# Kernel tuning notes

Measured on AMD Instinct MI355X. Metric: run time of the kernel, lower is better.

Reference implementation:

```python
import math
import jax, jax.numpy as jnp
import numpy as np

D_MODEL = 1024
NUM_HEADS = 16
HEAD_DIM = D_MODEL // NUM_HEADS
THETA = 10000.0
MAX_SEQ_LEN = 2048
BATCH = 4
SEQ = 2048


def _rope_tables():
    # angles[i, j] = i / theta**(2j/d_k), shapes [max_seq_len, head_dim//2]
    i = jnp.arange(MAX_SEQ_LEN, dtype=jnp.float32)
    k = jnp.arange(0, HEAD_DIM, 2, dtype=jnp.float32) / HEAD_DIM
    angles = i[:, None] * (1.0 / (THETA ** k))[None, :]
    return jnp.cos(angles), jnp.sin(angles)


def _apply_rope(x, token_positions, cos_tab, sin_tab):
    # x: [b, h, s, d_k]; token_positions: [s]
    b, h, s, dk = x.shape
    xr = x.reshape(b, h, s, dk // 2, 2)
    x0, x1 = xr[..., 0], xr[..., 1]
    cos_pos = cos_tab[token_positions]  # [s, dk//2]
    sin_pos = sin_tab[token_positions]
    x0_rot = x0 * cos_pos - x1 * sin_pos
    x1_rot = x0 * sin_pos + x1 * cos_pos
    return jnp.stack([x0_rot, x1_rot], axis=-1).reshape(x.shape)


def setup_inputs() -> dict:
    key = jax.random.key(0)
    k1, k2, k3 = jax.random.split(key, 3)
    std_qkv = math.sqrt(2.0 / (D_MODEL + 3 * D_MODEL))
    std_o = math.sqrt(2.0 / (D_MODEL + D_MODEL))
    return {
        "x": jax.random.normal(k1, (BATCH, SEQ, D_MODEL), dtype=jnp.float32),
        "token_positions": jnp.arange(SEQ, dtype=jnp.int64) if jax.config.jax_enable_x64 else jnp.arange(SEQ, dtype=jnp.int32),
        "qkv_w": jax.random.normal(k2, (3 * D_MODEL, D_MODEL), dtype=jnp.float32) * std_qkv,
        "o_w": jax.random.normal(k3, (D_MODEL, D_MODEL), dtype=jnp.float32) * std_o,
    }


def reference(x, token_positions, qkv_w, o_w):
    b, s, _ = x.shape
    cos_tab, sin_tab = _rope_tables()
    # fused QKV projection: [b, s, 3*d_model]
    qkv = jnp.einsum('bsd,ed->bse', x, qkv_w)
    qkv = qkv.reshape(b, s, 3, NUM_HEADS, HEAD_DIM)
    q = jnp.transpose(qkv[:, :, 0], (0, 2, 1, 3))  # [b, h, s, hd]
    k = jnp.transpose(qkv[:, :, 1], (0, 2, 1, 3))
    v = jnp.transpose(qkv[:, :, 2], (0, 2, 1, 3))
    q = _apply_rope(q, token_positions, cos_tab, sin_tab)
    k = _apply_rope(k, token_positions, cos_tab, sin_tab)
    # causal mask and eager softmax attention (full [b,h,s,s] scores)
    scores = jnp.einsum('bhnk,bhmk->bhnm', q, k) / math.sqrt(HEAD_DIM)
    causal = jnp.tril(jnp.ones((s, s), dtype=bool))
    scores = jnp.where(causal, scores, -jnp.inf)
    attn = jax.nn.softmax(scores, axis=-1)
    ctx = jnp.einsum('bhnm,bhmv->bhnv', attn, v)
    ctx = jnp.transpose(ctx, (0, 2, 1, 3)).reshape(b, s, D_MODEL)
    return jnp.einsum('bsd,ed->bse', ctx, o_w)
```

## Files before the change

### kernel.cpp

```cpp
#include <hip/hip_runtime.h>


#define DM   1024
#define NH   16
#define HD   64
#define SEQL 2048
#define BATCH 4
#define QKV_ELEMS 8388608

using short8 = __attribute__((ext_vector_type(8))) short;
using f32x4  = __attribute__((ext_vector_type(4))) float;
typedef unsigned short u16;

#define WAIT_VM(n) __builtin_amdgcn_s_waitcnt(0x0F70 | (n))
#define BARRIER()  __builtin_amdgcn_s_barrier()

__device__ __forceinline__ u16 f2bf(float f) {
    unsigned u = __builtin_bit_cast(unsigned, f);
    u += 0x7fffu + ((u >> 16) & 1u);
    return (u16)(u >> 16);
}
__device__ __forceinline__ float bf2f(u16 h) {
    unsigned u = ((unsigned)h) << 16;
    return __builtin_bit_cast(float, u);
}
__device__ __forceinline__ unsigned pk2bf(float a, float b) {
    return (unsigned)f2bf(a) | ((unsigned)f2bf(b) << 16);
}
__device__ __forceinline__ float fexp2(float x) {
#if __has_builtin(__builtin_amdgcn_exp2f)
    return __builtin_amdgcn_exp2f(x);
#else
    return __expf(x * 0.6931471805599453f);
#endif
}

__device__ __forceinline__ void load16(const void* g, void* l) {
    __builtin_amdgcn_global_load_lds(
        (__attribute__((address_space(1))) unsigned int*)(unsigned long long)g,
        (__attribute__((address_space(3))) unsigned int*)(unsigned int)(unsigned long long)l,
        16, 0, 0);
}

__global__ __launch_bounds__(256) void prep(const float* __restrict__ x, u16* __restrict__ xb,
                                            const float* __restrict__ qw, u16* __restrict__ wb,
                                            const float* __restrict__ ow, u16* __restrict__ owb,
                                            float* __restrict__ cost, float* __restrict__ sint) {
    int bx = blockIdx.x;
    if (bx < 12288) {
        const float* in; u16* out; int i;
        if (bx < 8192)       { in = x;  out = xb;  i = bx * 256 + threadIdx.x; }
        else if (bx < 11264) { in = qw; out = wb;  i = (bx - 8192) * 256 + threadIdx.x; }
        else                 { in = ow; out = owb; i = (bx - 11264) * 256 + threadIdx.x; }
        float4 v = ((const float4*)in)[i];
        uint2 o;
        o.x = pk2bf(v.x, v.y);
        o.y = pk2bf(v.z, v.w);
        ((uint2*)out)[i] = o;
    } else {
        int t = (bx - 12288) * 256 + threadIdx.x;
        int j = t & 31, pos = t >> 5;
        float freq = exp2f((float)j * (-2.0f / 64.0f) * 13.287712379549449f);
        float ang = (float)pos * freq;
        cost[t] = cosf(ang);
        sint[t] = sinf(ang);
    }
}

__device__ __forceinline__ void gemm128_core(const u16* __restrict__ A,
                                             const u16* __restrict__ B,
                                             int K, int m0, int n0,
                                             u16* As, u16* Bs, f32x4 acc[4][4]) {
    int tid = threadIdx.x, w = tid >> 6, l = tid & 63;
    int l15 = l & 15, l4 = l >> 4;
    int wm = w >> 1, wn = w & 1;
    int r0 = 32 * w + (l >> 2);
    int gblk = ((l & 3) ^ ((l >> 4) & 3)) * 8;
    const u16* gA0 = A + (size_t)(m0 + r0) * K + gblk;
    const u16* gA1 = gA0 + (size_t)16 * K;
    const u16* gB0 = B + (size_t)(n0 + r0) * K + gblk;
    const u16* gB1 = gB0 + (size_t)16 * K;
    char* ldsA = (char*)As + 2048 * w;
    char* ldsB = (char*)Bs + 2048 * w;
    int fo = ((l4 ^ (l15 >> 2)) & 3) * 16;
    f32x4 z = {0.f, 0.f, 0.f, 0.f};
#pragma unroll
    for (int i = 0; i < 4; ++i)
#pragma unroll
        for (int j = 0; j < 4; ++j) acc[i][j] = z;
    int nk = K >> 5;
#pragma unroll
    for (int t = 0; t < 2; ++t) {
        int ko = t << 5, nb = t * 8192;
        load16(gA0 + ko, ldsA + nb); load16(gA1 + ko, ldsA + nb + 1024);
        load16(gB0 + ko, ldsB + nb); load16(gB1 + ko, ldsB + nb + 1024);
    }
    int buf = 0;
    for (int kt = 0; kt < nk; ++kt) {
        if (kt < nk - 1) WAIT_VM(4); else WAIT_VM(0);
        BARRIER();
        if (kt + 2 < nk) {
            int ko = (kt + 2) << 5;
            int nb = 8192 * ((buf + 2) % 3);
            load16(gA0 + ko, ldsA + nb); load16(gA1 + ko, ldsA + nb + 1024);
            load16(gB0 + ko, ldsB + nb); load16(gB1 + ko, ldsB + nb + 1024);
        }
        const char* bA = (const char*)As + 8192 * buf;
        const char* bB = (const char*)Bs + 8192 * buf;
        short8 a[4], b[4];
#pragma unroll
        for (int i = 0; i < 4; ++i)
            a[i] = *(const short8*)(bA + (64 * wm + 16 * i + l15) * 64 + fo);
#pragma unroll
        for (int j = 0; j < 4; ++j)
            b[j] = *(const short8*)(bB + (64 * wn + 16 * j + l15) * 64 + fo);
#pragma unroll
        for (int i = 0; i < 4; ++i)
#pragma unroll
            for (int j = 0; j < 4; ++j)
                acc[i][j] = __builtin_amdgcn_mfma_f32_16x16x32_bf16(a[i], b[j], acc[i][j], 0, 0, 0);
        buf = (buf + 1) % 3;
    }
}

__global__ __launch_bounds__(256) void gemm_qkv(const u16* __restrict__ xb,
                                                const u16* __restrict__ wb,
                                                u16* __restrict__ qkv,
                                                u16* __restrict__ vt) {
    __shared__ __align__(16) u16 As[3 * 128 * 32], Bs[3 * 128 * 32];
    f32x4 acc[4][4];
    int m0 = blockIdx.y * 128, n0 = blockIdx.x * 128;
    gemm128_core(xb, wb, DM, m0, n0, As, Bs, acc);
    int l = threadIdx.x & 63, w = threadIdx.x >> 6;
    int l15 = l & 15, l4 = l >> 4;
    int wm = w >> 1, wn = w & 1;
    if (blockIdx.x >= 16) {
#pragma unroll
        for (int j = 0; j < 4; ++j) {
            int nV = (n0 - 2048) + 64 * wn + 16 * j + l15;
            int h = nV >> 6, d = nV & 63;
#pragma unroll
            for (int i = 0; i < 4; ++i) {
                int sb = m0 + 64 * wm + 16 * i + 4 * l4;
                int b = sb >> 11, s = sb & 2047;
                uint2 pk;
                pk.x = pk2bf(acc[i][j][0], acc[i][j][1]);
                pk.y = pk2bf(acc[i][j][2], acc[i][j][3]);
                *(uint2*)&vt[((size_t)(b * 16 + h) * HD + d) * SEQL + s] = pk;
            }
        }
    } else {
#pragma unroll
        for (int j = 0; j < 4; ++j) {
            int n = n0 + 64 * wn + 16 * j + l15;
            int which = n >> 10, h = (n >> 6) & 15, d = n & 63;
            u16* base = qkv + (size_t)which * QKV_ELEMS;
#pragma unroll
            for (int i = 0; i < 4; ++i) {
#pragma unroll
                for (int r = 0; r < 4; ++r) {
                    int m = m0 + 64 * wm + 16 * i + 4 * l4 + r;
                    int b = m >> 11, s = m & 2047;
                    base[((size_t)(b * 16 + h) * SEQL + s) * HD + d] = f2bf(acc[i][j][r]);
                }
            }
        }
    }
}

__global__ __launch_bounds__(256) void gemm_out(const u16* __restrict__ ctx,
                                                const u16* __restrict__ owb,
                                                float* __restrict__ out) {
    __shared__ __align__(16) u16 As[3 * 128 * 32], Bs[3 * 128 * 32];
    f32x4 acc[4][4];
    int m0 = blockIdx.y * 128, n0 = blockIdx.x * 128;
    gemm128_core(ctx, owb, DM, m0, n0, As, Bs, acc);
    int l = threadIdx.x & 63, w = threadIdx.x >> 6;
    int l15 = l & 15, l4 = l >> 4;
    int wm = w >> 1, wn = w & 1;
#pragma unroll
    for (int i = 0; i < 4; ++i) {
        int mb = m0 + 64 * wm + 16 * i + 4 * l4;
#pragma unroll
        for (int j = 0; j < 4; ++j) {
            int n = n0 + 64 * wn + 16 * j + l15;
#pragma unroll
            for (int r = 0; r < 4; ++r)
                out[(size_t)(mb + r) * DM + n] = acc[i][j][r];
        }
    }
}

__global__ __launch_bounds__(256) void rope_apply(unsigned int* __restrict__ qk,
                                                  const int* __restrict__ pos_ids,
                                                  const float* __restrict__ cost,
                                                  const float* __restrict__ sint) {
    int t = blockIdx.x * 256 + threadIdx.x;
    uint2 v = ((const uint2*)qk)[t];
    int pe = 2 * t;
    int d2 = pe & 31, s = (pe >> 5) & 2047;
    int pos = pos_ids[s];
    float sc = (pe < QKV_ELEMS / 2) ? 0.18033688011112042f : 1.0f;
    float2 cc = *(const float2*)&cost[pos * 32 + d2];
    float2 ss = *(const float2*)&sint[pos * 32 + d2];
    float x0 = bf2f((u16)(v.x & 0xffffu)), x1 = bf2f((u16)(v.x >> 16));
    float y0 = bf2f((u16)(v.y & 0xffffu)), y1 = bf2f((u16)(v.y >> 16));
    uint2 o;
    o.x = pk2bf((x0 * cc.x - x1 * ss.x) * sc, (x0 * ss.x + x1 * cc.x) * sc);
    o.y = pk2bf((y0 * cc.y - y1 * ss.y) * sc, (y0 * ss.y + y1 * cc.y) * sc);
    ((uint2*)qk)[t] = o;
}

__device__ __forceinline__ void flash_pass(int qt, const u16* __restrict__ Qb,
                                           const u16* __restrict__ Kb,
                                           const u16* __restrict__ Vb,
                                           u16* __restrict__ ctx, int bh,
                                           u16* KsB, u16* VsB, u16* PsB) {
    int tid = threadIdx.x, w = tid >> 6, l = tid & 63;
    int l15 = l & 15, l4 = l >> 4;
    int q0 = qt * 128;
    int swz = l15 & 7;
    int b0 = (l4 ^ swz) * 16;

    const u16* qr = Qb + (size_t)(q0 + 16 * w + l15) * HD;
    short8 aq0 = *(const short8*)&qr[l4 * 8];
    short8 aq1 = *(const short8*)&qr[32 + l4 * 8];

    int srow = l >> 3;
    int sblk = ((l & 7) ^ srow) * 8;
    const u16* gK = Kb + (size_t)(8 * w + srow) * HD + sblk;
    const u16* gV = Vb + (size_t)(8 * w + srow) * SEQL + sblk;
    char* ldsK = (char*)KsB + 1024 * w;
    char* ldsV = (char*)VsB + 1024 * w;
    char* prow = (char*)PsB + 2048 * w + l15 * 128;

    f32x4 z = {0.f, 0.f, 0.f, 0.f};
    f32x4 O[4] = {z, z, z, z};
    float lsum = 0.f;
    int nk = 2 * qt + 2;
    int rowlim = 16 * (w & 3) + l15;

    BARRIER();
#pragma unroll
    for (int t = 0; t < 2; ++t) {
        load16(gK + (size_t)(t * 64) * HD, ldsK + t * 8192);
        load16(gV + t * 64,                ldsV + t * 8192);
    }
    int buf = 0;
    for (int it = 0; it < nk; ++it) {
        if (it < nk - 1) WAIT_VM(2); else WAIT_VM(0);
        BARRIER();
        if (it + 2 < nk) {
            int k0n = (it + 2) * 64;
            int nb = 8192 * ((buf + 2) % 3);
            load16(gK + (size_t)k0n * HD, ldsK + nb);
            load16(gV + k0n,              ldsV + nb);
        }
        if (!(w < 4 && it == nk - 1)) {
            const char* bK = (const char*)KsB + 8192 * buf;
            const char* bV = (const char*)VsB + 8192 * buf;
            short8 kf[4][2], vf[4][2];
#pragma unroll
            for (int c = 0; c < 4; ++c) {
                const char* kr = bK + (16 * c + l15) * 128;
                kf[c][0] = *(const short8*)(kr + b0);
                kf[c][1] = *(const short8*)(kr + (b0 ^ 64));
                const char* vr = bV + (16 * c + l15) * 128;
                vf[c][0] = *(const short8*)(vr + b0);
                vf[c][1] = *(const short8*)(vr + (b0 ^ 64));
            }
            f32x4 S[4];
#pragma unroll
            for (int c = 0; c < 4; ++c) {
                S[c] = __builtin_amdgcn_mfma_f32_16x16x32_bf16(kf[c][0], aq0, z, 0, 0, 0);
                S[c] = __builtin_amdgcn_mfma_f32_16x16x32_bf16(kf[c][1], aq1, S[c], 0, 0, 0);
            }
            bool diag = (it == nk - 2 + (w >> 2));
            if (diag) {
#pragma unroll
                for (int c = 0; c < 4; ++c)
#pragma unroll
                    for (int r = 0; r < 4; ++r)
                        if (16 * c + 4 * l4 + r > rowlim) S[c][r] = -3e38f;
            }
#pragma unroll
            for (int c = 0; c < 4; ++c)
#pragma unroll
                for (int r = 0; r < 4; ++r) {
                    float p = fexp2(S[c][r]);
                    S[c][r] = p;
                    lsum += p;
                }
#pragma unroll
            for (int c = 0; c < 4; ++c) {
                uint2 pk;
                pk.x = pk2bf(S[c][0], S[c][1]);
                pk.y = pk2bf(S[c][2], S[c][3]);
                *(uint2*)(prow + ((((2 * c + (l4 >> 1)) ^ swz) << 4) | ((l4 & 1) << 3))) = pk;
            }
            short8 ap0 = *(const short8*)(prow + b0);
            short8 ap1 = *(const short8*)(prow + (b0 ^ 64));
#pragma unroll
            for (int nt = 0; nt < 4; ++nt) {
                O[nt] = __builtin_amdgcn_mfma_f32_16x16x32_bf16(ap0, vf[nt][0], O[nt], 0, 0, 0);
                O[nt] = __builtin_amdgcn_mfma_f32_16x16x32_bf16(ap1, vf[nt][1], O[nt], 0, 0, 0);
            }
        }
        buf = (buf + 1) % 3;
    }
    lsum += __shfl_xor(lsum, 16);
    lsum += __shfl_xor(lsum, 32);
    float linv[4];
#pragma unroll
    for (int r = 0; r < 4; ++r) linv[r] = 1.0f / __shfl(lsum, 20 * l4 + r);
    int b = bh >> 4, h = bh & 15;
#pragma unroll
    for (int nt = 0; nt < 4; ++nt) {
        int d = 16 * nt + l15;
#pragma unroll
        for (int r = 0; r < 4; ++r) {
            int s = q0 + 16 * w + 4 * l4 + r;
            ctx[((size_t)(b * SEQL + s)) * DM + h * 64 + d] = f2bf(O[nt][r] * linv[r]);
        }
    }
}

__global__ __launch_bounds__(512, 4) void flash_attn(const u16* __restrict__ Q,
                                                     const u16* __restrict__ K,
                                                     const u16* __restrict__ Vt,
                                                     u16* __restrict__ ctx) {
    __shared__ __align__(16) u16 Ks[3][64 * 64];
    __shared__ __align__(16) u16 Vs[3][64 * 64];
    __shared__ __align__(16) u16 Ps[8][16 * 64];
    int bh = blockIdx.y, pair = blockIdx.x;
    const u16* Qb = Q + (size_t)bh * SEQL * HD;
    const u16* Kb = K + (size_t)bh * SEQL * HD;
    const u16* Vb = Vt + (size_t)bh * HD * SEQL;
    flash_pass(15 - pair, Qb, Kb, Vb, ctx, bh, &Ks[0][0], &Vs[0][0], &Ps[0][0]);
    flash_pass(pair,      Qb, Kb, Vb, ctx, bh, &Ks[0][0], &Vs[0][0], &Ps[0][0]);
}

extern "C" void kernel_launch(void* const* d_in, const int* in_sizes, int n_in,
                              void* d_out, int out_size, void* d_ws, size_t ws_size,
                              hipStream_t stream) {
    const float* x     = (const float*)d_in[0];
    const int*   pos   = (const int*)d_in[1];
    const float* qkv_w = (const float*)d_in[2];
    const float* o_w   = (const float*)d_in[3];
    float* out = (float*)d_out;

    char* ws = (char*)d_ws;
    u16*   xb   = (u16*)(ws);
    u16*   wb   = (u16*)(ws + 16777216);
    u16*   owb  = (u16*)(ws + 23068672);
    float* cost = (float*)(ws + 25165824);
    float* sint = (float*)(ws + 25427968);
    u16*   qkv  = (u16*)(ws + 25690112);
    u16*   vt   = (u16*)(ws + 76021760);
    u16*   ctx  = xb;

    prep<<<12544, 256, 0, stream>>>(x, xb, qkv_w, wb, o_w, owb, cost, sint);
    gemm_qkv<<<dim3(24, 64), 256, 0, stream>>>(xb, wb, qkv, vt);
    rope_apply<<<16384, 256, 0, stream>>>((unsigned int*)qkv, pos, cost, sint);
    flash_attn<<<dim3(8, 64), 512, 0, stream>>>(qkv, qkv + QKV_ELEMS, vt, ctx);
    gemm_out<<<dim3(8, 64), 256, 0, stream>>>(ctx, owb, out);
}
```

Before: 256.7 us.

## Fuse RoPE into QKV GEMM epilogue and process two query tiles per attention pass

Drops the separate rope_apply kernel and applies the rotation plus the softmax scale to Q/K inside the QKV GEMM epilogue, using a lane shuffle to fetch each element's pair partner. This removes one full read-modify-write pass over Q and K. The flash attention pass now handles two 128-row query groups per 256-row tile, so each loaded K/V tile is reused twice. This halves the grid and lowers the occupancy hint to 2, which raises register pressure and reduces parallelism.

```diff
diff --git a/kernel.cpp b/kernel.cpp
--- a/kernel.cpp
+++ b/kernel.cpp
@@ -126,7 +126,10 @@
 __global__ __launch_bounds__(256) void gemm_qkv(const u16* __restrict__ xb,
                                                 const u16* __restrict__ wb,
                                                 u16* __restrict__ qkv,
-                                                u16* __restrict__ vt) {
+                                                u16* __restrict__ vt,
+                                                const int* __restrict__ pos_ids,
+                                                const float* __restrict__ cost,
+                                                const float* __restrict__ sint) {
     __shared__ __align__(16) u16 As[3 * 128 * 32], Bs[3 * 128 * 32];
     f32x4 acc[4][4];
     int m0 = blockIdx.y * 128, n0 = blockIdx.x * 128;
@@ -150,10 +153,12 @@
             }
         }
     } else {
+        float sc = (blockIdx.x < 8) ? 0.18033688011112042f : 1.0f;
 #pragma unroll
         for (int j = 0; j < 4; ++j) {
             int n = n0 + 64 * wn + 16 * j + l15;
             int which = n >> 10, h = (n >> 6) & 15, d = n & 63;
+            int d2 = d >> 1;
             u16* base = qkv + (size_t)which * QKV_ELEMS;
 #pragma unroll
             for (int i = 0; i < 4; ++i) {
@@ -161,7 +166,13 @@
                 for (int r = 0; r < 4; ++r) {
                     int m = m0 + 64 * wm + 16 * i + 4 * l4 + r;
                     int b = m >> 11, s = m & 2047;
-                    base[((size_t)(b * 16 + h) * SEQL + s) * HD + d] = f2bf(acc[i][j][r]);
+                    int pos = pos_ids[s];
+                    float c  = cost[pos * 32 + d2];
+                    float sn = sint[pos * 32 + d2];
+                    float v  = acc[i][j][r];
+                    float vp = __shfl_xor(v, 1);
+                    float o  = (d & 1) ? (vp * sn + v * c) : (v * c - vp * sn);
+                    base[((size_t)(b * 16 + h) * SEQL + s) * HD + d] = f2bf(o * sc);
                 }
             }
         }
@@ -191,26 +202,6 @@
     }
 }
 
-__global__ __launch_bounds__(256) void rope_apply(unsigned int* __restrict__ qk,
-                                                  const int* __restrict__ pos_ids,
-                                                  const float* __restrict__ cost,
-                                                  const float* __restrict__ sint) {
-    int t = blockIdx.x * 256 + threadIdx.x;
-    uint2 v = ((const uint2*)qk)[t];
-    int pe = 2 * t;
-    int d2 = pe & 31, s = (pe >> 5) & 2047;
-    int pos = pos_ids[s];
-    float sc = (pe < QKV_ELEMS / 2) ? 0.18033688011112042f : 1.0f;
-    float2 cc = *(const float2*)&cost[pos * 32 + d2];
-    float2 ss = *(const float2*)&sint[pos * 32 + d2];
-    float x0 = bf2f((u16)(v.x & 0xffffu)), x1 = bf2f((u16)(v.x >> 16));
-    float y0 = bf2f((u16)(v.y & 0xffffu)), y1 = bf2f((u16)(v.y >> 16));
-    uint2 o;
-    o.x = pk2bf((x0 * cc.x - x1 * ss.x) * sc, (x0 * ss.x + x1 * cc.x) * sc);
-    o.y = pk2bf((y0 * cc.y - y1 * ss.y) * sc, (y0 * ss.y + y1 * cc.y) * sc);
-    ((uint2*)qk)[t] = o;
-}
-
 __device__ __forceinline__ void flash_pass(int qt, const u16* __restrict__ Qb,
                                            const u16* __restrict__ Kb,
                                            const u16* __restrict__ Vb,
@@ -218,14 +209,17 @@
                                            u16* KsB, u16* VsB, u16* PsB) {
     int tid = threadIdx.x, w = tid >> 6, l = tid & 63;
     int l15 = l & 15, l4 = l >> 4;
-    int q0 = qt * 128;
+    int q0 = qt * 256;
     int swz = l15 & 7;
     int b0 = (l4 ^ swz) * 16;
 
-    const u16* qr = Qb + (size_t)(q0 + 16 * w + l15) * HD;
-    short8 aq0 = *(const short8*)&qr[l4 * 8];
-    short8 aq1 = *(const short8*)&qr[32 + l4 * 8];
-
+    short8 aq[2][2];
+#pragma unroll
+    for (int g = 0; g < 2; ++g) {
+        const u16* qr = Qb + (size_t)(q0 + 128 * g + 16 * w + l15) * HD;
+        aq[g][0] = *(const short8*)&qr[l4 * 8];
+        aq[g][1] = *(const short8*)&qr[32 + l4 * 8];
+    }
     int srow = l >> 3;
     int sblk = ((l & 7) ^ srow) * 8;
     const u16* gK = Kb + (size_t)(8 * w + srow) * HD + sblk;
@@ -235,9 +229,10 @@
     char* prow = (char*)PsB + 2048 * w + l15 * 128;
 
     f32x4 z = {0.f, 0.f, 0.f, 0.f};
-    f32x4 O[4] = {z, z, z, z};
-    float lsum = 0.f;
-    int nk = 2 * qt + 2;
+    f32x4 O[2][4] = {{z, z, z, z}, {z, z, z, z}};
+    float lsum[2] = {0.f, 0.f};
+    int nk = 4 * qt + 4;
+    int d0 = 4 * qt + (w >> 2);
     int rowlim = 16 * (w & 3) + l15;
 
     BARRIER();
@@ -256,7 +251,7 @@
             load16(gK + (size_t)k0n * HD, ldsK + nb);
             load16(gV + k0n,              ldsV + nb);
         }
-        if (!(w < 4 && it == nk - 1)) {
+        if (it <= d0 + 2) {
             const char* bK = (const char*)KsB + 8192 * buf;
             const char* bV = (const char*)VsB + 8192 * buf;
             short8 kf[4][2], vf[4][2];
@@ -269,63 +264,71 @@
                 vf[c][0] = *(const short8*)(vr + b0);
                 vf[c][1] = *(const short8*)(vr + (b0 ^ 64));
             }
-            f32x4 S[4];
-#pragma unroll
-            for (int c = 0; c < 4; ++c) {
-                S[c] = __builtin_amdgcn_mfma_f32_16x16x32_bf16(kf[c][0], aq0, z, 0, 0, 0);
-                S[c] = __builtin_amdgcn_mfma_f32_16x16x32_bf16(kf[c][1], aq1, S[c], 0, 0, 0);
-            }
-            bool diag = (it == nk - 2 + (w >> 2));
-            if (diag) {
+#pragma unroll
+            for (int g = 0; g < 2; ++g) {
+                int dg = d0 + 2 * g;
+                if (it > dg) continue;
+                f32x4 S[4];
+#pragma unroll
+                for (int c = 0; c < 4; ++c) {
+                    S[c] = __builtin_amdgcn_mfma_f32_16x16x32_bf16(kf[c][0], aq[g][0], z, 0, 0, 0);
+                    S[c] = __builtin_amdgcn_mfma_f32_16x16x32_bf16(kf[c][1], aq[g][1], S[c], 0, 0, 0);
+                }
+                if (it == dg) {
+#pragma unroll
+                    for (int c = 0; c < 4; ++c)
+#pragma unroll
+                        for (int r = 0; r < 4; ++r)
+                            if (16 * c + 4 * l4 + r > rowlim) S[c][r] = -3e38f;
+                }
 #pragma unroll
                 for (int c = 0; c < 4; ++c)
 #pragma unroll
-                    for (int r = 0; r < 4; ++r)
-                        if (16 * c + 4 * l4 + r > rowlim) S[c][r] = -3e38f;
-            }
-#pragma unroll
-            for (int c = 0; c < 4; ++c)
-#pragma unroll
-                for (int r = 0; r < 4; ++r) {
-                    float p = fexp2(S[c][r]);
-                    S[c][r] = p;
-                    lsum += p;
-                }
-#pragma unroll
-            for (int c = 0; c < 4; ++c) {
-                uint2 pk;
-                pk.x = pk2bf(S[c][0], S[c][1]);
-                pk.y = pk2bf(S[c][2], S[c][3]);
-                *(uint2*)(prow + ((((2 * c + (l4 >> 1)) ^ swz) << 4) | ((l4 & 1) << 3))) = pk;
-            }
-            short8 ap0 = *(const short8*)(prow + b0);
-            short8 ap1 = *(const short8*)(prow + (b0 ^ 64));
-#pragma unroll
-            for (int nt = 0; nt < 4; ++nt) {
-                O[nt] = __builtin_amdgcn_mfma_f32_16x16x32_bf16(ap0, vf[nt][0], O[nt], 0, 0, 0);
-                O[nt] = __builtin_amdgcn_mfma_f32_16x16x32_bf16(ap1, vf[nt][1], O[nt], 0, 0, 0);
+                    for (int r = 0; r < 4; ++r) {
+                        float p = fexp2(S[c][r]);
+                        S[c][r] = p;
+                        lsum[g] += p;
+                    }
+#pragma unroll
+                for (int c = 0; c < 4; ++c) {
+                    uint2 pk;
+                    pk.x = pk2bf(S[c][0], S[c][1]);
+                    pk.y = pk2bf(S[c][2], S[c][3]);
+                    *(uint2*)(prow + ((((2 * c + (l4 >> 1)) ^ swz) << 4) | ((l4 & 1) << 3))) = pk;
+                }
+                short8 ap0 = *(const short8*)(prow + b0);
+                short8 ap1 = *(const short8*)(prow + (b0 ^ 64));
+#pragma unroll
+                for (int nt = 0; nt < 4; ++nt) {
+                    O[g][nt] = __builtin_amdgcn_mfma_f32_16x16x32_bf16(ap0, vf[nt][0], O[g][nt], 0, 0, 0);
+                    O[g][nt] = __builtin_amdgcn_mfma_f32_16x16x32_bf16(ap1, vf[nt][1], O[g][nt], 0, 0, 0);
+                }
             }
         }
         buf = (buf + 1) % 3;
     }
-    lsum += __shfl_xor(lsum, 16);
-    lsum += __shfl_xor(lsum, 32);
-    float linv[4];
-#pragma unroll
-    for (int r = 0; r < 4; ++r) linv[r] = 1.0f / __shfl(lsum, 20 * l4 + r);
     int b = bh >> 4, h = bh & 15;
 #pragma unroll
-    for (int nt = 0; nt < 4; ++nt) {
-        int d = 16 * nt + l15;
-#pragma unroll
-        for (int r = 0; r < 4; ++r) {
-            int s = q0 + 16 * w + 4 * l4 + r;
-            ctx[((size_t)(b * SEQL + s)) * DM + h * 64 + d] = f2bf(O[nt][r] * linv[r]);
-        }
-    }
-}
-
-__global__ __launch_bounds__(512, 4) void flash_attn(const u16* __restrict__ Q,
+    for (int g = 0; g < 2; ++g) {
+        float ls = lsum[g];
+        ls += __shfl_xor(ls, 16);
+        ls += __shfl_xor(ls, 32);
+        float linv[4];
+#pragma unroll
+        for (int r = 0; r < 4; ++r) linv[r] = 1.0f / __shfl(ls, 20 * l4 + r);
+#pragma unroll
+        for (int nt = 0; nt < 4; ++nt) {
+            int d = 16 * nt + l15;
+#pragma unroll
+            for (int r = 0; r < 4; ++r) {
+                int s = q0 + 128 * g + 16 * w + 4 * l4 + r;
+                ctx[((size_t)(b * SEQL + s)) * DM + h * 64 + d] = f2bf(O[g][nt][r] * linv[r]);
+            }
+        }
+    }
+}
+
+__global__ __launch_bounds__(512, 2) void flash_attn(const u16* __restrict__ Q,
                                                      const u16* __restrict__ K,
                                                      const u16* __restrict__ Vt,
                                                      u16* __restrict__ ctx) {
@@ -336,8 +339,8 @@
     const u16* Qb = Q + (size_t)bh * SEQL * HD;
     const u16* Kb = K + (size_t)bh * SEQL * HD;
     const u16* Vb = Vt + (size_t)bh * HD * SEQL;
-    flash_pass(15 - pair, Qb, Kb, Vb, ctx, bh, &Ks[0][0], &Vs[0][0], &Ps[0][0]);
-    flash_pass(pair,      Qb, Kb, Vb, ctx, bh, &Ks[0][0], &Vs[0][0], &Ps[0][0]);
+    flash_pass(7 - pair, Qb, Kb, Vb, ctx, bh, &Ks[0][0], &Vs[0][0], &Ps[0][0]);
+    flash_pass(pair,     Qb, Kb, Vb, ctx, bh, &Ks[0][0], &Vs[0][0], &Ps[0][0]);
 }
 
 extern "C" void kernel_launch(void* const* d_in, const int* in_sizes, int n_in,
@@ -360,8 +363,7 @@
     u16*   ctx  = xb;
 
     prep<<<12544, 256, 0, stream>>>(x, xb, qkv_w, wb, o_w, owb, cost, sint);
-    gemm_qkv<<<dim3(24, 64), 256, 0, stream>>>(xb, wb, qkv, vt);
-    rope_apply<<<16384, 256, 0, stream>>>((unsigned int*)qkv, pos, cost, sint);
-    flash_attn<<<dim3(8, 64), 512, 0, stream>>>(qkv, qkv + QKV_ELEMS, vt, ctx);
+    gemm_qkv<<<dim3(24, 64), 256, 0, stream>>>(xb, wb, qkv, vt, pos, cost, sint);
+    flash_attn<<<dim3(4, 64), 512, 0, stream>>>(qkv, qkv + QKV_ELEMS, vt, ctx);
     gemm_out<<<dim3(8, 64), 256, 0, stream>>>(ctx, owb, out);
 }
```

Measured after the change: 247.8 us. 1.04x faster.
